# Performance work log

Hardware: AMD Instinct MI355X
Metric: run time of the kernel (lower is better)

## Reference

```python
import math
import jax, jax.numpy as jnp
import numpy as np

D_MODEL = 1024
NUM_HEADS = 16
D_K = D_MODEL // NUM_HEADS
RANK = 16
B, L = 2, 2048


def setup_inputs() -> dict:
    key = jax.random.key(0)
    ks = jax.random.split(key, 10)
    w_scale = 0.02  # keep activations well-scaled like trained linears
    return {
        "x_q": jax.random.normal(ks[0], (B, L, D_MODEL), jnp.float32),
        "x_kv": jax.random.normal(ks[1], (B, L, D_MODEL), jnp.float32),
        "Wq": jax.random.normal(ks[2], (D_MODEL, D_MODEL), jnp.float32) * w_scale,
        "bq": jnp.zeros((D_MODEL,), jnp.float32),
        "Wk": jax.random.normal(ks[3], (D_MODEL, D_MODEL), jnp.float32) * w_scale,
        "bk": jnp.zeros((D_MODEL,), jnp.float32),
        "Wv": jax.random.normal(ks[4], (D_MODEL, D_MODEL), jnp.float32) * w_scale,
        "bv": jnp.zeros((D_MODEL,), jnp.float32),
        "Wo": jax.random.normal(ks[5], (D_MODEL, D_MODEL), jnp.float32) * w_scale,
        "bo": jnp.zeros((D_MODEL,), jnp.float32),
        "U_bil": jax.random.normal(ks[6], (NUM_HEADS, D_K, RANK), jnp.float32) * 0.02,
        "V_bil": jax.random.normal(ks[7], (NUM_HEADS, D_K, RANK), jnp.float32) * 0.02,
        "padding_mask": jnp.zeros((B, L), bool),  # True = padded KV position
    }


def reference(x_q, x_kv, Wq, bq, Wk, bk, Wv, bv, Wo, bo, U_bil, V_bil, padding_mask):
    b, l, _ = x_q.shape
    # torch nn.Linear: y = x @ W.T + b
    Q = (x_q @ Wq.T + bq).reshape(b, l, NUM_HEADS, D_K).transpose(0, 2, 1, 3)  # [B,H,L,dk]
    K = (x_kv @ Wk.T + bk).reshape(b, l, NUM_HEADS, D_K).transpose(0, 2, 1, 3)
    V = (x_kv @ Wv.T + bv).reshape(b, l, NUM_HEADS, D_K).transpose(0, 2, 1, 3)
    # low-rank bilinear projections: [B,H,L,rank]
    Q_proj = jnp.einsum("bhld,hdr->bhlr", Q, U_bil)
    K_proj = jnp.einsum("bhld,hdr->bhlr", K, V_bil)
    scores = jnp.einsum("bhqr,bhkr->bhqk", Q_proj, K_proj) / math.sqrt(RANK)  # [B,H,L,L]
    scores = jnp.where(padding_mask[:, None, None, :], jnp.float32(-10000.0), scores)
    attn = jax.nn.softmax(scores, axis=-1)  # dropout is identity in eval mode
    ctx = jnp.einsum("bhqk,bhkd->bhqd", attn, V)
    ctx = ctx.transpose(0, 2, 1, 3).reshape(b, l, D_MODEL)
    return ctx @ Wo.T + bo
```

## Files before the change

### kernel.cpp

```cpp
#include <hip/hip_runtime.h>
#include <hip/hip_bf16.h>

#define DM   1024
#define NH   16
#define DK   64
#define RK   16
#define BB   2
#define LL   2048
#define TT   (BB*LL)
#define NSPL 2


typedef float f4   __attribute__((ext_vector_type(4)));
typedef float f2   __attribute__((ext_vector_type(2)));
typedef float f16v __attribute__((ext_vector_type(16)));
typedef short s8v  __attribute__((ext_vector_type(8)));
typedef unsigned int u2v __attribute__((ext_vector_type(2)));
typedef unsigned int u4v __attribute__((ext_vector_type(4)));

static __device__ __forceinline__ unsigned short f2b(float f) {
  __hip_bfloat16 h = __float2bfloat16(f);
  unsigned short u;
  __builtin_memcpy(&u, &h, 2);
  return u;
}
static __device__ __forceinline__ float b2f(unsigned short u) {
  __hip_bfloat16 h;
  __builtin_memcpy(&h, &u, 2);
  return __bfloat162float(h);
}

static __device__ __forceinline__ void gld_lds16(const void* g, void* l) {
  __builtin_amdgcn_global_load_lds(
      (const __attribute__((address_space(1))) unsigned int*)g,
      (__attribute__((address_space(3))) unsigned int*)l, 16, 0, 0);
}

static __device__ __forceinline__ void wait_vm0_barrier() {
  asm volatile("s_waitcnt vmcnt(0)" ::: "memory");
  __builtin_amdgcn_s_barrier();
}

static __device__ __forceinline__ void cast_rng(
    const float* __restrict__ s, unsigned short* __restrict__ d,
    int n4, int lb, int nb, int tid) {
  for (int i = lb*256 + tid; i < n4; i += nb*256) {
    const float4 v = ((const float4*)s)[i];
    ushort4 o;
    o.x = f2b(v.x); o.y = f2b(v.y); o.z = f2b(v.z); o.w = f2b(v.w);
    ((ushort4*)d)[i] = o;
  }
}

__global__ __launch_bounds__(256) void prep_k(
    const float* __restrict__ xq,  const float* __restrict__ xkv,
    const float* __restrict__ Wv,  const float* __restrict__ Wo,
    unsigned short* __restrict__ xq_b,  unsigned short* __restrict__ xkv_b,
    unsigned short* __restrict__ Wv_b,  unsigned short* __restrict__ Wo_b,
    const float* __restrict__ Wq,  const float* __restrict__ Wk,
    const float* __restrict__ Uq,  const float* __restrict__ Uk,
    unsigned short* __restrict__ Aq, unsigned short* __restrict__ Ak,
    const float* __restrict__ bq,  const float* __restrict__ bk,
    float* __restrict__ bpq, float* __restrict__ bpk) {
  __shared__ float sh[64*16 + 4*64];
  const int x = blockIdx.x, tid = threadIdx.x;
  if (x < 1024) {
    cast_rng(xq,  xq_b,  TT*DM/4, x,        1024, tid);
  } else if (x < 2048) {
    cast_rng(xkv, xkv_b, TT*DM/4, x - 1024, 1024, tid);
  } else if (x < 2304) {
    cast_rng(Wv,  Wv_b,  DM*DM/4, x - 2048, 256, tid);
  } else if (x < 2560) {
    cast_rng(Wo,  Wo_b,  DM*DM/4, x - 2304, 256, tid);
  } else if (x < 3072) {
    const int fidx = x - 2560;
    const int sel = fidx >> 8, f = fidx & 255;
    const float* W = sel ? Wk : Wq;
    const float* U = sel ? Uk : Uq;
    unsigned short* At = sel ? Ak : Aq;
    const float qs = sel ? 1.f : 0.25f;
    const int i0 = (f & 15) * 64, h = f >> 4;
    float* Us = sh;
    float* Ws = sh + 1024;
    const int il = tid & 63, rr = tid >> 6;
    for (int t = tid; t < 64*16; t += 256)
      Us[t] = U[(size_t)(h*DK + (t >> 4))*RK + (t & 15)];
    float acc[4] = {};
    for (int d0 = 0; d0 < DK; d0 += 4) {
      __syncthreads();
      Ws[rr*64 + il] = W[(size_t)(h*DK + d0 + rr)*DM + i0 + il];
      __syncthreads();
#pragma unroll
      for (int dd = 0; dd < 4; ++dd) {
        const float w = Ws[dd*64 + il];
#pragma unroll
        for (int j = 0; j < 4; ++j)
          acc[j] += w * Us[(d0 + dd)*16 + rr*4 + j];
      }
    }
#pragma unroll
    for (int j = 0; j < 4; ++j)
      At[(size_t)(h*RK + rr*4 + j)*DM + i0 + il] = f2b(acc[j] * qs);
  } else {
    const int h = tid >> 4, r = tid & 15;
    float aq = 0.f, ak = 0.f;
    for (int d = 0; d < DK; ++d) {
      aq += bq[h*DK + d] * Uq[(size_t)(h*DK + d)*RK + r];
      ak += bk[h*DK + d] * Uk[(size_t)(h*DK + d)*RK + r];
    }
    bpq[tid] = aq * 0.25f; bpk[tid] = ak;
  }
}

__global__ __launch_bounds__(256) void proj_k(
    const unsigned short* __restrict__ xq_b, const unsigned short* __restrict__ xkv_b,
    const unsigned short* __restrict__ Atq,  const unsigned short* __restrict__ Atk,
    const float* __restrict__ bpq, const float* __restrict__ bpk,
    unsigned short* __restrict__ Qp, unsigned short* __restrict__ Kp,
    const unsigned short* __restrict__ Wv_b, const float* __restrict__ bv,
    unsigned short* __restrict__ Vt) {
  __shared__ __align__(16) unsigned short shm[16384];
  const int f = blockIdx.x, tid = threadIdx.x;
  const int wave = tid >> 6, lane = tid & 63;
  const int quad = lane >> 4, l15 = lane & 15;
  const int ar = tid >> 2, ac = (tid & 3) * 8;
  const f4 z = {0.f, 0.f, 0.f, 0.f};

  if (f < 256) {
    const int xb = f & 63, yb = (f >> 6) & 1, zb = f >> 7;
    const unsigned short* Ag = zb ? xkv_b : xq_b;
    const unsigned short* Bg = zb ? Atk : Atq;
    const float* bias = zb ? bpk : bpq;
    unsigned short* C = zb ? Kp : Qp;
    unsigned short* Xs = shm;
    unsigned short* Bq = shm + 4096;
    const int t0 = xb*64, n0 = yb*128, nh = wave*32;
    f4 acc[4][2];
#pragma unroll
    for (int a = 0; a < 4; ++a) { acc[a][0] = z; acc[a][1] = z; }

    auto STAGE = [&](int buf, int k0) {
      gld_lds16(&Ag[(size_t)(t0 + ar)*DM + k0 + ac],      &Xs[buf*2048 + wave*512]);
      gld_lds16(&Bg[(size_t)(n0 + ar)*DM + k0 + ac],      &Bq[buf*4096 + wave*512]);
      gld_lds16(&Bg[(size_t)(n0 + 64 + ar)*DM + k0 + ac], &Bq[buf*4096 + 2048 + wave*512]);
    };
    STAGE(0, 0);
    wait_vm0_barrier();
    int cur = 0;
    for (int k0 = 0; k0 < DM; k0 += 32) {
      if (k0 + 32 < DM) STAGE(cur ^ 1, k0 + 32);
      s8v af[4], bf[2];
#pragma unroll
      for (int ms = 0; ms < 4; ++ms)
        af[ms] = *(const s8v*)&Xs[cur*2048 + (ms*16 + l15)*32 + quad*8];
#pragma unroll
      for (int ns = 0; ns < 2; ++ns)
        bf[ns] = *(const s8v*)&Bq[cur*4096 + (nh + ns*16 + l15)*32 + quad*8];
#pragma unroll
      for (int ms = 0; ms < 4; ++ms)
#pragma unroll
        for (int ns = 0; ns < 2; ++ns)
          acc[ms][ns] = __builtin_amdgcn_mfma_f32_16x16x32_bf16(
              af[ms], bf[ns], acc[ms][ns], 0, 0, 0);
      wait_vm0_barrier();
      cur ^= 1;
    }
#pragma unroll
    for (int ms = 0; ms < 4; ++ms) {
      const int tb = t0 + ms*16 + quad*4;
#pragma unroll
      for (int ns = 0; ns < 2; ++ns) {
        const int o = n0 + nh + ns*16 + l15;
        const float bvv = bias[o];
        f4 a = acc[ms][ns];
#pragma unroll
        for (int rg = 0; rg < 4; ++rg) {
          const int tt = tb + rg;
          C[(((size_t)(tt >> 11)*NH + (o >> 4))*LL + (tt & 2047))*RK + (o & 15)]
              = f2b(a[rg] + bvv);
        }
      }
    }
  } else {
    const int g = f - 256, gx = g & 31, gy = g >> 5;
    unsigned short* As = shm;
    unsigned short* Bs = shm + 8192;
    const int t0 = gx*128, n0 = gy*128;
    f4 acc[2][8];
#pragma unroll
    for (int m = 0; m < 2; ++m)
#pragma unroll
      for (int n = 0; n < 8; ++n) acc[m][n] = z;

    auto STAGE = [&](int buf, int k0) {
      gld_lds16(&xkv_b[(size_t)(t0 + ar)*DM + k0 + ac],      &As[buf*4096 + wave*512]);
      gld_lds16(&xkv_b[(size_t)(t0 + 64 + ar)*DM + k0 + ac], &As[buf*4096 + 2048 + wave*512]);
      gld_lds16(&Wv_b[(size_t)(n0 + ar)*DM + k0 + ac],       &Bs[buf*4096 + wave*512]);
      gld_lds16(&Wv_b[(size_t)(n0 + 64 + ar)*DM + k0 + ac],  &Bs[buf*4096 + 2048 + wave*512]);
    };
    STAGE(0, 0);
    wait_vm0_barrier();
    int cur = 0;
    for (int k0 = 0; k0 < DM; k0 += 32) {
      if (k0 + 32 < DM) STAGE(cur ^ 1, k0 + 32);
      s8v af[2], bf[8];
#pragma unroll
      for (int ms = 0; ms < 2; ++ms)
        af[ms] = *(const s8v*)&As[cur*4096 + (wave*32 + ms*16 + l15)*32 + quad*8];
#pragma unroll
      for (int ns = 0; ns < 8; ++ns)
        bf[ns] = *(const s8v*)&Bs[cur*4096 + (ns*16 + l15)*32 + quad*8];
#pragma unroll
      for (int ms = 0; ms < 2; ++ms)
#pragma unroll
        for (int ns = 0; ns < 8; ++ns)
          acc[ms][ns] = __builtin_amdgcn_mfma_f32_16x16x32_bf16(
              af[ms], bf[ns], acc[ms][ns], 0, 0, 0);
      wait_vm0_barrier();
      cur ^= 1;
    }
#pragma unroll
    for (int ms = 0; ms < 2; ++ms) {
      const int tb = t0 + wave*32 + ms*16 + quad*4;
#pragma unroll
      for (int ns = 0; ns < 8; ++ns) {
        const int o = n0 + ns*16 + l15;
        const float bvv = bv[o];
        f4 a = acc[ms][ns];
        const int bb = tb >> 11, l = tb & 2047;
        ushort4 pk;
        pk.x = f2b(a[0] + bvv); pk.y = f2b(a[1] + bvv);
        pk.z = f2b(a[2] + bvv); pk.w = f2b(a[3] + bvv);
        *(ushort4*)&Vt[((size_t)bb*DM + o)*LL + l] = pk;
      }
    }
  }
}

template<bool MASKED>
static __device__ __forceinline__ void softmax_pack(
    const f16v& s0, const f16v& s1, const unsigned long long mb, const int hi,
    f2& den2, unsigned int (&Pd)[2][4][2]) {
  const f2 neg1 = {-1.f, -1.f};
#pragma unroll
  for (int nt = 0; nt < 2; ++nt) {
    const f16v& sv = nt ? s1 : s0;
#pragma unroll
    for (int r = 0; r < 4; ++r) {
#pragma unroll
      for (int jp = 0; jp < 2; ++jp) {
        f2 em2;
        em2[0] = __expf(sv[r*4 + jp*2]);
        em2[1] = __expf(sv[r*4 + jp*2 + 1]);
        if (MASKED) {
          const int kl = nt*32 + jp*2 + 8*r + 4*hi;
          if ((mb >> kl) & 1ull)       em2[0] = 0.f;
          if ((mb >> (kl + 1)) & 1ull) em2[1] = 0.f;
        }
        f2 ep2;
        asm("v_pk_add_f32 %0, %1, %2" : "=v"(ep2) : "v"(em2), "v"(neg1));
        asm("v_pk_add_f32 %0, %0, %1" : "+v"(den2) : "v"(ep2));
        asm("v_cvt_pk_bf16_f32 %0, %1, %2"
            : "=v"(Pd[nt][r][jp]) : "v"(ep2[0]), "v"(ep2[1]));
      }
    }
  }
}

__global__ __launch_bounds__(256, 4) void attn_k(
    const unsigned short* __restrict__ Qp, const unsigned short* __restrict__ Kp,
    const unsigned short* __restrict__ Vt,
    const unsigned char* __restrict__ msk,
    unsigned short* __restrict__ P, float* __restrict__ denP,
    float* __restrict__ Vsum) {
  __shared__ __align__(16) unsigned short Ks[2][2][65][8];
  __shared__ __align__(16) unsigned short Vs[2][8][65][8];
  const int tid = threadIdx.x;

  if (blockIdx.z == 4) {
    if (blockIdx.y >= BB) return;
    const int h = blockIdx.x, b = blockIdx.y;
    const int d = tid >> 2, part = tid & 3;
    const unsigned short* row = Vt + ((size_t)b*DM + h*DK + d)*LL + part*512;
    float s = 0.f;
    for (int i = 0; i < 512; i += 8) {
      const s8v v = *(const s8v*)&row[i];
#pragma unroll
      for (int j = 0; j < 8; ++j) s += b2f((unsigned short)v[j]);
    }
    s += __shfl_xor(s, 1);
    s += __shfl_xor(s, 2);
    if (part == 0) Vsum[((size_t)b*NH + h)*DK + d] = s;
    return;
  }

  const int q0 = blockIdx.x * 128, h = blockIdx.y;
  const int b = blockIdx.z & (BB - 1), ksp = blockIdx.z >> 1;
  const int kbeg = ksp * (LL / NSPL);
  const int NT = (LL / NSPL) / 64;
  const int w = tid >> 6, lane = tid & 63;
  const int l31 = lane & 31, hi = lane >> 5;

  const s8v qfrag = *(const s8v*)&Qp[
      (((size_t)b*NH + h)*LL + q0 + w*32 + l31)*RK + hi*8];

  const int sr = tid >> 2, sp = tid & 3;
  const unsigned short* __restrict__ Vrow =
      Vt + ((size_t)b*DM + h*DK + sr)*LL + kbeg;
  const unsigned short* __restrict__ Kbase =
      Kp + (((size_t)b*NH + h)*LL + kbeg + sr)*RK + sp*4;
  const unsigned char*  __restrict__ Mrow = msk + (size_t)b*LL + kbeg + lane;

  u2v kpre; s8v vpre0, vpre1;
  unsigned char mcur, mnext;

  kpre  = *(const u2v*)&Kbase[0];
  vpre0 = *(const s8v*)&Vrow[sp*16];
  vpre1 = *(const s8v*)&Vrow[sp*16 + 8];
  mcur  = Mrow[0];
  *(u2v*)&Ks[0][sp>>1][sr][(sp&1)*4] = kpre;
  *(s8v*)&Vs[0][sp*2][sr][0]   = vpre0;
  *(s8v*)&Vs[0][sp*2+1][sr][0] = vpre1;
  kpre  = *(const u2v*)&Kbase[(size_t)64*RK];
  vpre0 = *(const s8v*)&Vrow[64 + sp*16];
  vpre1 = *(const s8v*)&Vrow[64 + sp*16 + 8];
  mnext = Mrow[64];
  __syncthreads();

  f16v acc0, acc1, z16;
#pragma unroll
  for (int i = 0; i < 16; ++i) { acc0[i] = 0.f; acc1[i] = 0.f; z16[i] = 0.f; }
  f2 den2 = {0.f, 0.f};

  for (int t = 0; t < NT; ++t) {
    const int cur = t & 1;
    const unsigned long long mb = __ballot(mcur != 0);

    const s8v kf0 = *(const s8v*)&Ks[cur][hi][l31][0];
    const s8v kf1 = *(const s8v*)&Ks[cur][hi][32 + l31][0];

    const f16v s0 = __builtin_amdgcn_mfma_f32_32x32x16_bf16(kf0, qfrag, z16, 0, 0, 0);
    const f16v s1 = __builtin_amdgcn_mfma_f32_32x32x16_bf16(kf1, qfrag, z16, 0, 0, 0);

    unsigned int Pd[2][4][2];
    if (__builtin_expect(mb != 0ull, 0))
      softmax_pack<true >(s0, s1, mb, hi, den2, Pd);
    else
      softmax_pack<false>(s0, s1, mb, hi, den2, Pd);

#pragma unroll
    for (int kc = 0; kc < 4; ++kc) {
      const int nt = kc >> 1, a = (kc & 1)*2;
      const u2v r0 = __builtin_amdgcn_permlane32_swap(
          Pd[nt][a][0], Pd[nt][a+1][0], false, false);
      const u2v r1 = __builtin_amdgcn_permlane32_swap(
          Pd[nt][a][1], Pd[nt][a+1][1], false, false);
      u4v efi;
      efi[0] = r0[0];
      efi[1] = r1[0];
      efi[2] = r0[1];
      efi[3] = r1[1];
      const s8v ef = __builtin_bit_cast(s8v, efi);
      const s8v vf0 = *(const s8v*)&Vs[cur][kc*2 + hi][l31][0];
      const s8v vf1 = *(const s8v*)&Vs[cur][kc*2 + hi][32 + l31][0];
      acc0 = __builtin_amdgcn_mfma_f32_32x32x16_bf16(ef, vf0, acc0, 0, 0, 0);
      acc1 = __builtin_amdgcn_mfma_f32_32x32x16_bf16(ef, vf1, acc1, 0, 0, 0);
    }

    if (t + 1 < NT) {
      *(u2v*)&Ks[cur^1][sp>>1][sr][(sp&1)*4] = kpre;
      *(s8v*)&Vs[cur^1][sp*2][sr][0]   = vpre0;
      *(s8v*)&Vs[cur^1][sp*2+1][sr][0] = vpre1;
      const int tn = (t + 2 < NT) ? t + 2 : NT - 1;
      kpre  = *(const u2v*)&Kbase[(size_t)tn*64*RK];
      vpre0 = *(const s8v*)&Vrow[tn*64 + sp*16];
      vpre1 = *(const s8v*)&Vrow[tn*64 + sp*16 + 8];
      mcur  = mnext;
      mnext = Mrow[tn*64];
    }
    __syncthreads();
  }

  float den = den2[0] + den2[1] + (float)(32 * NT);
  den += __shfl_xor(den, 32);
  if (hi == 0)
    denP[(((size_t)ksp*BB + b)*NH + h)*LL + q0 + w*32 + l31] = den;

#pragma unroll
  for (int rg = 0; rg < 16; ++rg) {
    const int qr = (rg & 3) + 8*(rg >> 2) + 4*hi;
    const size_t pbase =
        ((size_t)ksp*TT + b*LL + q0 + w*32 + qr)*DM + h*DK;
    P[pbase + l31]      = f2b(acc0[rg]);
    P[pbase + 32 + l31] = f2b(acc1[rg]);
  }
}

__global__ __launch_bounds__(256) void outred_k(
    const unsigned short* __restrict__ P, const float* __restrict__ Vsum,
    const float* __restrict__ denP, const unsigned short* __restrict__ Bg,
    const float* __restrict__ bias, float* __restrict__ C) {
  __shared__ __align__(16) unsigned short P0s[2][2048];
  __shared__ __align__(16) unsigned short P1s[2][2048];
  __shared__ __align__(16) unsigned short Bs[2][4096];
  __shared__ float vsS[1024];
  __shared__ float invS[64][16];
  const int f = blockIdx.x;
  const int t0 = (f & 63) * 64, n0 = (f >> 6) * 128;
  const int tid = threadIdx.x, wave = tid >> 6, lane = tid & 63;
  const int quad = lane >> 4, l15 = lane & 15;
  const int nh = wave * 32;
  const int ar = tid >> 2, ac = (tid & 3) * 8;
  const int trow = t0 + ar;
  const int b = t0 >> 11;

  for (int i = tid; i < 1024; i += 256)
    vsS[i] = Vsum[(size_t)b*DM + i];
  {
    const int r = tid >> 2, h0 = (tid & 3) * 4;
    const int lr = (t0 + r) & 2047;
#pragma unroll
    for (int j = 0; j < 4; ++j) {
      const int h = h0 + j;
      const float dn = denP[((size_t)b*NH + h)*LL + lr] +
                       denP[(((size_t)BB + b)*NH + h)*LL + lr];
      invS[r][h] = 1.f / fmaxf(dn, 1e-30f);
    }
  }

  auto STAGE = [&](int buf, int k0) {
    gld_lds16(&P[(size_t)trow*DM + k0 + ac],             &P0s[buf][wave*512]);
    gld_lds16(&P[((size_t)TT + trow)*DM + k0 + ac],      &P1s[buf][wave*512]);
    gld_lds16(&Bg[(size_t)(n0 + ar)*DM + k0 + ac],       &Bs[buf][wave*512]);
    gld_lds16(&Bg[(size_t)(n0 + 64 + ar)*DM + k0 + ac],  &Bs[buf][2048 + wave*512]);
  };
  STAGE(0, 0);
  asm volatile("s_waitcnt vmcnt(0) lgkmcnt(0)" ::: "memory");
  __builtin_amdgcn_s_barrier();

  const f4 z = {0.f, 0.f, 0.f, 0.f};
  f4 acc[4][2];
#pragma unroll
  for (int a = 0; a < 4; ++a) { acc[a][0] = z; acc[a][1] = z; }

  int cur = 0;
  for (int k0 = 0; k0 < DM; k0 += 32) {
    if (k0 + 32 < DM) STAGE(cur ^ 1, k0 + 32);
    const int hk = k0 >> 6;
    const f4 vq0 = *(const f4*)&vsS[k0 + quad*8];
    const f4 vq1 = *(const f4*)&vsS[k0 + quad*8 + 4];
    s8v af[4], bf[2];
#pragma unroll
    for (int ms = 0; ms < 4; ++ms) {
      const int r16 = ms*16 + l15;
      const float inv = invS[r16][hk];
      const s8v p0 = *(const s8v*)&P0s[cur][r16*32 + quad*8];
      const s8v p1 = *(const s8v*)&P1s[cur][r16*32 + quad*8];
      float e[8];
#pragma unroll
      for (int j = 0; j < 4; ++j) {
        e[j]     = (vq0[j] + b2f((unsigned short)p0[j])
                           + b2f((unsigned short)p1[j])) * inv;
        e[4 + j] = (vq1[j] + b2f((unsigned short)p0[4+j])
                           + b2f((unsigned short)p1[4+j])) * inv;
      }
      unsigned int d0, d1, d2, d3;
      asm("v_cvt_pk_bf16_f32 %0, %1, %2" : "=v"(d0) : "v"(e[0]), "v"(e[1]));
      asm("v_cvt_pk_bf16_f32 %0, %1, %2" : "=v"(d1) : "v"(e[2]), "v"(e[3]));
      asm("v_cvt_pk_bf16_f32 %0, %1, %2" : "=v"(d2) : "v"(e[4]), "v"(e[5]));
      asm("v_cvt_pk_bf16_f32 %0, %1, %2" : "=v"(d3) : "v"(e[6]), "v"(e[7]));
      u4v efi; efi[0] = d0; efi[1] = d1; efi[2] = d2; efi[3] = d3;
      af[ms] = __builtin_bit_cast(s8v, efi);
    }
#pragma unroll
    for (int ns = 0; ns < 2; ++ns)
      bf[ns] = *(const s8v*)&Bs[cur][(nh + ns*16 + l15)*32 + quad*8];
#pragma unroll
    for (int ms = 0; ms < 4; ++ms)
#pragma unroll
      for (int ns = 0; ns < 2; ++ns)
        acc[ms][ns] = __builtin_amdgcn_mfma_f32_16x16x32_bf16(
            af[ms], bf[ns], acc[ms][ns], 0, 0, 0);
    wait_vm0_barrier();
    cur ^= 1;
  }

#pragma unroll
  for (int ms = 0; ms < 4; ++ms) {
    const int tb = t0 + ms*16 + quad*4;
#pragma unroll
    for (int ns = 0; ns < 2; ++ns) {
      const int o = n0 + nh + ns*16 + l15;
      const float bv = bias[o];
      f4 a = acc[ms][ns];
#pragma unroll
      for (int rg = 0; rg < 4; ++rg)
        C[(size_t)(tb + rg)*DM + o] = a[rg] + bv;
    }
  }
}

extern "C" void kernel_launch(void* const* d_in, const int* in_sizes, int n_in,
                              void* d_out, int out_size, void* d_ws, size_t ws_size,
                              hipStream_t stream) {
  (void)in_sizes; (void)n_in; (void)out_size; (void)ws_size;
  const float* x_q   = (const float*)d_in[0];
  const float* x_kv  = (const float*)d_in[1];
  const float* Wq    = (const float*)d_in[2];
  const float* bq    = (const float*)d_in[3];
  const float* Wk    = (const float*)d_in[4];
  const float* bk    = (const float*)d_in[5];
  const float* Wv    = (const float*)d_in[6];
  const float* bv    = (const float*)d_in[7];
  const float* Wo    = (const float*)d_in[8];
  const float* bo    = (const float*)d_in[9];
  const float* U_bil = (const float*)d_in[10];
  const float* V_bil = (const float*)d_in[11];
  const unsigned char* pmask = (const unsigned char*)d_in[12];
  float* out = (float*)d_out;

  char* w = (char*)d_ws;
  unsigned short* xq_b  = (unsigned short*)(w);
  unsigned short* xkv_b = (unsigned short*)(w +  8388608);
  unsigned short* Wv_b  = (unsigned short*)(w + 16777216);
  unsigned short* Wo_b  = (unsigned short*)(w + 18874368);
  unsigned short* Atq   = (unsigned short*)(w + 20971520);
  unsigned short* Atk   = (unsigned short*)(w + 21495808);
  float*          bpq   = (float*)(w + 22020096);
  float*          bpk   = (float*)(w + 22021120);
  unsigned short* Qp    = (unsigned short*)(w + 22022144);
  unsigned short* Kp    = (unsigned short*)(w + 24119296);
  unsigned short* Vt    = (unsigned short*)(w + 26216448);
  float*          Vsum  = (float*)(w + 34605056);
  float*          denP  = (float*)(w + 34613248);
  unsigned short* Pbuf  = (unsigned short*)w;

  prep_k<<<3073, 256, 0, stream>>>(
      x_q, x_kv, Wv, Wo, xq_b, xkv_b, Wv_b, Wo_b,
      Wq, Wk, U_bil, V_bil, Atq, Atk, bq, bk, bpq, bpk);
  proj_k<<<512, 256, 0, stream>>>(
      xq_b, xkv_b, Atq, Atk, bpq, bpk, Qp, Kp, Wv_b, bv, Vt);
  attn_k<<<dim3(LL/128, NH, 5), 256, 0, stream>>>(
      Qp, Kp, Vt, pmask, Pbuf, denP, Vsum);
  outred_k<<<512, 256, 0, stream>>>(Pbuf, Vsum, denP, Wo_b, bo, out);
}
```

Before: 227.3 us.

## Fuse all stages into one cooperative persistent kernel with grid syncs

Merges the four kernels (cast/prep, projection, attention, output reduction) into a single cooperative kernel of 1024 blocks separated by grid.sync(), with a multi-launch fallback. The aim is to remove launch gaps and tail effects between stages. To fit four blocks per CU it drops the double-buffered LDS staging in favour of single-buffer loads with two __syncthreads per k-step. It also retiles the V projection to 64x128 tiles, switches softmax to raw v_exp_f32 with the log2e factor folded into the Q scale, and transposes the denominator layout so it can be read as vectors.

```diff
diff --git a/kernel.cpp b/kernel.cpp
--- a/kernel.cpp
+++ b/kernel.cpp
@@ -1,5 +1,8 @@
 #include <hip/hip_runtime.h>
 #include <hip/hip_bf16.h>
+#include <hip/hip_cooperative_groups.h>
+
+namespace cg = cooperative_groups;
 
 #define DM   1024
 #define NH   16
@@ -18,6 +21,15 @@
 typedef unsigned int u2v __attribute__((ext_vector_type(2)));
 typedef unsigned int u4v __attribute__((ext_vector_type(4)));
 
+#define SMEM_BYTES 24576
+
+struct Args {
+  const float *xq, *xkv, *Wv, *Wo, *Wq, *Wk, *Uq, *Uk, *bq, *bk, *bv, *bo;
+  const unsigned char* msk;
+  unsigned short *xq_b, *xkv_b, *Wv_b, *Wo_b, *Atq, *Atk, *Qp, *Kp, *Vt, *P;
+  float *bpq, *bpk, *denP, *Vsum, *out;
+};
+
 static __device__ __forceinline__ unsigned short f2b(float f) {
   __hip_bfloat16 h = __float2bfloat16(f);
   unsigned short u;
@@ -29,6 +41,9 @@
   __builtin_memcpy(&h, &u, 2);
   return __bfloat162float(h);
 }
+static __device__ __forceinline__ float fexp2(float x) {
+  float r; asm("v_exp_f32 %0, %1" : "=v"(r) : "v"(x)); return r;
+}
 
 static __device__ __forceinline__ void gld_lds16(const void* g, void* l) {
   __builtin_amdgcn_global_load_lds(
@@ -36,52 +51,32 @@
       (__attribute__((address_space(3))) unsigned int*)l, 16, 0, 0);
 }
 
-static __device__ __forceinline__ void wait_vm0_barrier() {
-  asm volatile("s_waitcnt vmcnt(0)" ::: "memory");
-  __builtin_amdgcn_s_barrier();
-}
-
-static __device__ __forceinline__ void cast_rng(
-    const float* __restrict__ s, unsigned short* __restrict__ d,
-    int n4, int lb, int nb, int tid) {
-  for (int i = lb*256 + tid; i < n4; i += nb*256) {
-    const float4 v = ((const float4*)s)[i];
+#define QSCALE 0.36067376022224085f
+
+static __device__ void stage_prep(char* sm, int id, const Args& a) {
+  const int tid = threadIdx.x;
+  const int NF = TT*DM/4, NW = DM*DM/4;
+  const int TOTC = 2*NF + 2*NW;
+  for (int i = id*256 + tid; i < TOTC; i += 1024*256) {
+    const float* s; unsigned short* d; int off;
+    if (i < NF)           { s = a.xq;  d = a.xq_b;  off = i; }
+    else if (i < 2*NF)    { s = a.xkv; d = a.xkv_b; off = i - NF; }
+    else if (i < 2*NF+NW) { s = a.Wv;  d = a.Wv_b;  off = i - 2*NF; }
+    else                  { s = a.Wo;  d = a.Wo_b;  off = i - 2*NF - NW; }
+    const float4 v = ((const float4*)s)[off];
     ushort4 o;
     o.x = f2b(v.x); o.y = f2b(v.y); o.z = f2b(v.z); o.w = f2b(v.w);
-    ((ushort4*)d)[i] = o;
-  }
-}
-
-__global__ __launch_bounds__(256) void prep_k(
-    const float* __restrict__ xq,  const float* __restrict__ xkv,
-    const float* __restrict__ Wv,  const float* __restrict__ Wo,
-    unsigned short* __restrict__ xq_b,  unsigned short* __restrict__ xkv_b,
-    unsigned short* __restrict__ Wv_b,  unsigned short* __restrict__ Wo_b,
-    const float* __restrict__ Wq,  const float* __restrict__ Wk,
-    const float* __restrict__ Uq,  const float* __restrict__ Uk,
-    unsigned short* __restrict__ Aq, unsigned short* __restrict__ Ak,
-    const float* __restrict__ bq,  const float* __restrict__ bk,
-    float* __restrict__ bpq, float* __restrict__ bpk) {
-  __shared__ float sh[64*16 + 4*64];
-  const int x = blockIdx.x, tid = threadIdx.x;
-  if (x < 1024) {
-    cast_rng(xq,  xq_b,  TT*DM/4, x,        1024, tid);
-  } else if (x < 2048) {
-    cast_rng(xkv, xkv_b, TT*DM/4, x - 1024, 1024, tid);
-  } else if (x < 2304) {
-    cast_rng(Wv,  Wv_b,  DM*DM/4, x - 2048, 256, tid);
-  } else if (x < 2560) {
-    cast_rng(Wo,  Wo_b,  DM*DM/4, x - 2304, 256, tid);
-  } else if (x < 3072) {
-    const int fidx = x - 2560;
-    const int sel = fidx >> 8, f = fidx & 255;
-    const float* W = sel ? Wk : Wq;
-    const float* U = sel ? Uk : Uq;
-    unsigned short* At = sel ? Ak : Aq;
-    const float qs = sel ? 1.f : 0.25f;
+    ((ushort4*)d)[off] = o;
+  }
+  if (id < 512) {
+    const int sel = id >> 8, f = id & 255;
+    const float* W = sel ? a.Wk : a.Wq;
+    const float* U = sel ? a.Uk : a.Uq;
+    unsigned short* At = sel ? a.Atk : a.Atq;
+    const float qs = sel ? 1.f : QSCALE;
     const int i0 = (f & 15) * 64, h = f >> 4;
-    float* Us = sh;
-    float* Ws = sh + 1024;
+    float* Us = (float*)sm;
+    float* Ws = (float*)sm + 1024;
     const int il = tid & 63, rr = tid >> 6;
     for (int t = tid; t < 64*16; t += 256)
       Us[t] = U[(size_t)(h*DK + (t >> 4))*RK + (t & 15)];
@@ -101,69 +96,57 @@
 #pragma unroll
     for (int j = 0; j < 4; ++j)
       At[(size_t)(h*RK + rr*4 + j)*DM + i0 + il] = f2b(acc[j] * qs);
-  } else {
+  } else if (id == 512) {
     const int h = tid >> 4, r = tid & 15;
     float aq = 0.f, ak = 0.f;
     for (int d = 0; d < DK; ++d) {
-      aq += bq[h*DK + d] * Uq[(size_t)(h*DK + d)*RK + r];
-      ak += bk[h*DK + d] * Uk[(size_t)(h*DK + d)*RK + r];
-    }
-    bpq[tid] = aq * 0.25f; bpk[tid] = ak;
-  }
-}
-
-__global__ __launch_bounds__(256) void proj_k(
-    const unsigned short* __restrict__ xq_b, const unsigned short* __restrict__ xkv_b,
-    const unsigned short* __restrict__ Atq,  const unsigned short* __restrict__ Atk,
-    const float* __restrict__ bpq, const float* __restrict__ bpk,
-    unsigned short* __restrict__ Qp, unsigned short* __restrict__ Kp,
-    const unsigned short* __restrict__ Wv_b, const float* __restrict__ bv,
-    unsigned short* __restrict__ Vt) {
-  __shared__ __align__(16) unsigned short shm[16384];
-  const int f = blockIdx.x, tid = threadIdx.x;
+      aq += a.bq[h*DK + d] * a.Uq[(size_t)(h*DK + d)*RK + r];
+      ak += a.bk[h*DK + d] * a.Uk[(size_t)(h*DK + d)*RK + r];
+    }
+    a.bpq[tid] = aq * QSCALE;
+    a.bpk[tid] = ak;
+  }
+}
+
+static __device__ void stage_proj(char* sm, int id, const Args& a) {
+  if (id >= 768) return;
+  const int tid = threadIdx.x;
   const int wave = tid >> 6, lane = tid & 63;
   const int quad = lane >> 4, l15 = lane & 15;
   const int ar = tid >> 2, ac = (tid & 3) * 8;
   const f4 z = {0.f, 0.f, 0.f, 0.f};
-
-  if (f < 256) {
-    const int xb = f & 63, yb = (f >> 6) & 1, zb = f >> 7;
-    const unsigned short* Ag = zb ? xkv_b : xq_b;
-    const unsigned short* Bg = zb ? Atk : Atq;
-    const float* bias = zb ? bpk : bpq;
-    unsigned short* C = zb ? Kp : Qp;
-    unsigned short* Xs = shm;
-    unsigned short* Bq = shm + 4096;
+  unsigned short* Xs = (unsigned short*)sm;
+  unsigned short* Bs = (unsigned short*)(sm + 4096);
+
+  if (id < 256) {
+    const int xb = id & 63, yb = (id >> 6) & 1, zb = id >> 7;
+    const unsigned short* Ag = zb ? a.xkv_b : a.xq_b;
+    const unsigned short* Bg = zb ? a.Atk : a.Atq;
+    const float* bias = zb ? a.bpk : a.bpq;
+    unsigned short* C = zb ? a.Kp : a.Qp;
     const int t0 = xb*64, n0 = yb*128, nh = wave*32;
     f4 acc[4][2];
 #pragma unroll
-    for (int a = 0; a < 4; ++a) { acc[a][0] = z; acc[a][1] = z; }
-
-    auto STAGE = [&](int buf, int k0) {
-      gld_lds16(&Ag[(size_t)(t0 + ar)*DM + k0 + ac],      &Xs[buf*2048 + wave*512]);
-      gld_lds16(&Bg[(size_t)(n0 + ar)*DM + k0 + ac],      &Bq[buf*4096 + wave*512]);
-      gld_lds16(&Bg[(size_t)(n0 + 64 + ar)*DM + k0 + ac], &Bq[buf*4096 + 2048 + wave*512]);
-    };
-    STAGE(0, 0);
-    wait_vm0_barrier();
-    int cur = 0;
+    for (int q = 0; q < 4; ++q) { acc[q][0] = z; acc[q][1] = z; }
     for (int k0 = 0; k0 < DM; k0 += 32) {
-      if (k0 + 32 < DM) STAGE(cur ^ 1, k0 + 32);
+      __syncthreads();
+      gld_lds16(&Ag[(size_t)(t0 + ar)*DM + k0 + ac],      &Xs[wave*512]);
+      gld_lds16(&Bg[(size_t)(n0 + ar)*DM + k0 + ac],      &Bs[wave*512]);
+      gld_lds16(&Bg[(size_t)(n0 + 64 + ar)*DM + k0 + ac], &Bs[2048 + wave*512]);
+      __syncthreads();
       s8v af[4], bf[2];
 #pragma unroll
       for (int ms = 0; ms < 4; ++ms)
-        af[ms] = *(const s8v*)&Xs[cur*2048 + (ms*16 + l15)*32 + quad*8];
+        af[ms] = *(const s8v*)&Xs[(ms*16 + l15)*32 + quad*8];
 #pragma unroll
       for (int ns = 0; ns < 2; ++ns)
-        bf[ns] = *(const s8v*)&Bq[cur*4096 + (nh + ns*16 + l15)*32 + quad*8];
+        bf[ns] = *(const s8v*)&Bs[(nh + ns*16 + l15)*32 + quad*8];
 #pragma unroll
       for (int ms = 0; ms < 4; ++ms)
 #pragma unroll
         for (int ns = 0; ns < 2; ++ns)
           acc[ms][ns] = __builtin_amdgcn_mfma_f32_16x16x32_bf16(
               af[ms], bf[ns], acc[ms][ns], 0, 0, 0);
-      wait_vm0_barrier();
-      cur ^= 1;
     }
 #pragma unroll
     for (int ms = 0; ms < 4; ++ms) {
@@ -172,66 +155,54 @@
       for (int ns = 0; ns < 2; ++ns) {
         const int o = n0 + nh + ns*16 + l15;
         const float bvv = bias[o];
-        f4 a = acc[ms][ns];
+        f4 v = acc[ms][ns];
 #pragma unroll
         for (int rg = 0; rg < 4; ++rg) {
           const int tt = tb + rg;
           C[(((size_t)(tt >> 11)*NH + (o >> 4))*LL + (tt & 2047))*RK + (o & 15)]
-              = f2b(a[rg] + bvv);
+              = f2b(v[rg] + bvv);
         }
       }
     }
   } else {
-    const int g = f - 256, gx = g & 31, gy = g >> 5;
-    unsigned short* As = shm;
-    unsigned short* Bs = shm + 8192;
-    const int t0 = gx*128, n0 = gy*128;
-    f4 acc[2][8];
-#pragma unroll
-    for (int m = 0; m < 2; ++m)
-#pragma unroll
-      for (int n = 0; n < 8; ++n) acc[m][n] = z;
-
-    auto STAGE = [&](int buf, int k0) {
-      gld_lds16(&xkv_b[(size_t)(t0 + ar)*DM + k0 + ac],      &As[buf*4096 + wave*512]);
-      gld_lds16(&xkv_b[(size_t)(t0 + 64 + ar)*DM + k0 + ac], &As[buf*4096 + 2048 + wave*512]);
-      gld_lds16(&Wv_b[(size_t)(n0 + ar)*DM + k0 + ac],       &Bs[buf*4096 + wave*512]);
-      gld_lds16(&Wv_b[(size_t)(n0 + 64 + ar)*DM + k0 + ac],  &Bs[buf*4096 + 2048 + wave*512]);
-    };
-    STAGE(0, 0);
-    wait_vm0_barrier();
-    int cur = 0;
+    const int g = id - 256;
+    const int t0 = (g & 63)*64, n0 = (g >> 6)*128, nh = wave*32;
+    f4 acc[4][2];
+#pragma unroll
+    for (int q = 0; q < 4; ++q) { acc[q][0] = z; acc[q][1] = z; }
     for (int k0 = 0; k0 < DM; k0 += 32) {
-      if (k0 + 32 < DM) STAGE(cur ^ 1, k0 + 32);
-      s8v af[2], bf[8];
-#pragma unroll
-      for (int ms = 0; ms < 2; ++ms)
-        af[ms] = *(const s8v*)&As[cur*4096 + (wave*32 + ms*16 + l15)*32 + quad*8];
-#pragma unroll
-      for (int ns = 0; ns < 8; ++ns)
-        bf[ns] = *(const s8v*)&Bs[cur*4096 + (ns*16 + l15)*32 + quad*8];
-#pragma unroll
-      for (int ms = 0; ms < 2; ++ms)
-#pragma unroll
-        for (int ns = 0; ns < 8; ++ns)
+      __syncthreads();
+      gld_lds16(&a.xkv_b[(size_t)(t0 + ar)*DM + k0 + ac],     &Xs[wave*512]);
+      gld_lds16(&a.Wv_b[(size_t)(n0 + ar)*DM + k0 + ac],      &Bs[wave*512]);
+      gld_lds16(&a.Wv_b[(size_t)(n0 + 64 + ar)*DM + k0 + ac], &Bs[2048 + wave*512]);
+      __syncthreads();
+      s8v af[4], bf[2];
+#pragma unroll
+      for (int ms = 0; ms < 4; ++ms)
+        af[ms] = *(const s8v*)&Xs[(ms*16 + l15)*32 + quad*8];
+#pragma unroll
+      for (int ns = 0; ns < 2; ++ns)
+        bf[ns] = *(const s8v*)&Bs[(nh + ns*16 + l15)*32 + quad*8];
+#pragma unroll
+      for (int ms = 0; ms < 4; ++ms)
+#pragma unroll
+        for (int ns = 0; ns < 2; ++ns)
           acc[ms][ns] = __builtin_amdgcn_mfma_f32_16x16x32_bf16(
               af[ms], bf[ns], acc[ms][ns], 0, 0, 0);
-      wait_vm0_barrier();
-      cur ^= 1;
-    }
-#pragma unroll
-    for (int ms = 0; ms < 2; ++ms) {
-      const int tb = t0 + wave*32 + ms*16 + quad*4;
-#pragma unroll
-      for (int ns = 0; ns < 8; ++ns) {
-        const int o = n0 + ns*16 + l15;
-        const float bvv = bv[o];
-        f4 a = acc[ms][ns];
+    }
+#pragma unroll
+    for (int ms = 0; ms < 4; ++ms) {
+      const int tb = t0 + ms*16 + quad*4;
+#pragma unroll
+      for (int ns = 0; ns < 2; ++ns) {
+        const int o = n0 + nh + ns*16 + l15;
+        const float bvv = a.bv[o];
+        f4 v = acc[ms][ns];
         const int bb = tb >> 11, l = tb & 2047;
         ushort4 pk;
-        pk.x = f2b(a[0] + bvv); pk.y = f2b(a[1] + bvv);
-        pk.z = f2b(a[2] + bvv); pk.w = f2b(a[3] + bvv);
-        *(ushort4*)&Vt[((size_t)bb*DM + o)*LL + l] = pk;
+        pk.x = f2b(v[0] + bvv); pk.y = f2b(v[1] + bvv);
+        pk.z = f2b(v[2] + bvv); pk.w = f2b(v[3] + bvv);
+        *(ushort4*)&a.Vt[((size_t)bb*DM + o)*LL + l] = pk;
       }
     }
   }
@@ -250,8 +221,8 @@
 #pragma unroll
       for (int jp = 0; jp < 2; ++jp) {
         f2 em2;
-        em2[0] = __expf(sv[r*4 + jp*2]);
-        em2[1] = __expf(sv[r*4 + jp*2 + 1]);
+        em2[0] = fexp2(sv[r*4 + jp*2]);
+        em2[1] = fexp2(sv[r*4 + jp*2 + 1]);
         if (MASKED) {
           const int kl = nt*32 + jp*2 + 8*r + 4*hi;
           if ((mb >> kl) & 1ull)       em2[0] = 0.f;
@@ -267,49 +238,28 @@
   }
 }
 
-__global__ __launch_bounds__(256, 4) void attn_k(
-    const unsigned short* __restrict__ Qp, const unsigned short* __restrict__ Kp,
-    const unsigned short* __restrict__ Vt,
-    const unsigned char* __restrict__ msk,
-    unsigned short* __restrict__ P, float* __restrict__ denP,
-    float* __restrict__ Vsum) {
-  __shared__ __align__(16) unsigned short Ks[2][2][65][8];
-  __shared__ __align__(16) unsigned short Vs[2][8][65][8];
+static __device__ void stage_attn(char* sm, int id, const Args& a) {
   const int tid = threadIdx.x;
-
-  if (blockIdx.z == 4) {
-    if (blockIdx.y >= BB) return;
-    const int h = blockIdx.x, b = blockIdx.y;
-    const int d = tid >> 2, part = tid & 3;
-    const unsigned short* row = Vt + ((size_t)b*DM + h*DK + d)*LL + part*512;
-    float s = 0.f;
-    for (int i = 0; i < 512; i += 8) {
-      const s8v v = *(const s8v*)&row[i];
-#pragma unroll
-      for (int j = 0; j < 8; ++j) s += b2f((unsigned short)v[j]);
-    }
-    s += __shfl_xor(s, 1);
-    s += __shfl_xor(s, 2);
-    if (part == 0) Vsum[((size_t)b*NH + h)*DK + d] = s;
-    return;
-  }
-
-  const int q0 = blockIdx.x * 128, h = blockIdx.y;
-  const int b = blockIdx.z & (BB - 1), ksp = blockIdx.z >> 1;
+  auto Ks = (unsigned short (*)[2][65][8])sm;
+  auto Vs = (unsigned short (*)[8][65][8])(sm + 4160);
+
+  const int q0 = (id & 15) * 128, h = (id >> 4) & 15;
+  const int zz = id >> 8;
+  const int b = zz & (BB - 1), ksp = zz >> 1;
   const int kbeg = ksp * (LL / NSPL);
   const int NT = (LL / NSPL) / 64;
   const int w = tid >> 6, lane = tid & 63;
   const int l31 = lane & 31, hi = lane >> 5;
 
-  const s8v qfrag = *(const s8v*)&Qp[
+  const s8v qfrag = *(const s8v*)&a.Qp[
       (((size_t)b*NH + h)*LL + q0 + w*32 + l31)*RK + hi*8];
 
   const int sr = tid >> 2, sp = tid & 3;
   const unsigned short* __restrict__ Vrow =
-      Vt + ((size_t)b*DM + h*DK + sr)*LL + kbeg;
+      a.Vt + ((size_t)b*DM + h*DK + sr)*LL + kbeg;
   const unsigned short* __restrict__ Kbase =
-      Kp + (((size_t)b*NH + h)*LL + kbeg + sr)*RK + sp*4;
-  const unsigned char*  __restrict__ Mrow = msk + (size_t)b*LL + kbeg + lane;
+      a.Kp + (((size_t)b*NH + h)*LL + kbeg + sr)*RK + sp*4;
+  const unsigned char*  __restrict__ Mrow = a.msk + (size_t)b*LL + kbeg + lane;
 
   u2v kpre; s8v vpre0, vpre1;
   unsigned char mcur, mnext;
@@ -350,11 +300,11 @@
 
 #pragma unroll
     for (int kc = 0; kc < 4; ++kc) {
-      const int nt = kc >> 1, a = (kc & 1)*2;
+      const int nt = kc >> 1, aa = (kc & 1)*2;
       const u2v r0 = __builtin_amdgcn_permlane32_swap(
-          Pd[nt][a][0], Pd[nt][a+1][0], false, false);
+          Pd[nt][aa][0], Pd[nt][aa+1][0], false, false);
       const u2v r1 = __builtin_amdgcn_permlane32_swap(
-          Pd[nt][a][1], Pd[nt][a+1][1], false, false);
+          Pd[nt][aa][1], Pd[nt][aa+1][1], false, false);
       u4v efi;
       efi[0] = r0[0];
       efi[1] = r1[0];
@@ -384,30 +334,45 @@
   float den = den2[0] + den2[1] + (float)(32 * NT);
   den += __shfl_xor(den, 32);
   if (hi == 0)
-    denP[(((size_t)ksp*BB + b)*NH + h)*LL + q0 + w*32 + l31] = den;
+    a.denP[(((size_t)b*LL + q0 + w*32 + l31)*NSPL + ksp)*NH + h] = den;
 
 #pragma unroll
   for (int rg = 0; rg < 16; ++rg) {
     const int qr = (rg & 3) + 8*(rg >> 2) + 4*hi;
     const size_t pbase =
         ((size_t)ksp*TT + b*LL + q0 + w*32 + qr)*DM + h*DK;
-    P[pbase + l31]      = f2b(acc0[rg]);
-    P[pbase + 32 + l31] = f2b(acc1[rg]);
-  }
-}
-
-__global__ __launch_bounds__(256) void outred_k(
-    const unsigned short* __restrict__ P, const float* __restrict__ Vsum,
-    const float* __restrict__ denP, const unsigned short* __restrict__ Bg,
-    const float* __restrict__ bias, float* __restrict__ C) {
-  __shared__ __align__(16) unsigned short P0s[2][2048];
-  __shared__ __align__(16) unsigned short P1s[2][2048];
-  __shared__ __align__(16) unsigned short Bs[2][4096];
-  __shared__ float vsS[1024];
-  __shared__ float invS[64][16];
-  const int f = blockIdx.x;
-  const int t0 = (f & 63) * 64, n0 = (f >> 6) * 128;
-  const int tid = threadIdx.x, wave = tid >> 6, lane = tid & 63;
+    a.P[pbase + l31]      = f2b(acc0[rg]);
+    a.P[pbase + 32 + l31] = f2b(acc1[rg]);
+  }
+
+  if (id < 32) {
+    const int vh = id & 15, vb = id >> 4;
+    const int d = tid >> 2, part = tid & 3;
+    const unsigned short* row =
+        a.Vt + ((size_t)vb*DM + vh*DK + d)*LL + part*512;
+    float s = 0.f;
+    for (int i = 0; i < 512; i += 8) {
+      const s8v v = *(const s8v*)&row[i];
+#pragma unroll
+      for (int j = 0; j < 8; ++j) s += b2f((unsigned short)v[j]);
+    }
+    s += __shfl_xor(s, 1);
+    s += __shfl_xor(s, 2);
+    if (part == 0) a.Vsum[((size_t)vb*NH + vh)*DK + d] = s;
+  }
+}
+
+static __device__ void stage_outred(char* sm, int id, const Args& a) {
+  if (id >= 512) return;
+  const int tid = threadIdx.x;
+  unsigned short* P0s = (unsigned short*)sm;
+  unsigned short* P1s = (unsigned short*)(sm + 4096);
+  unsigned short* Bss = (unsigned short*)(sm + 8192);
+  float* vsS  = (float*)(sm + 16384);
+  float* invS = (float*)(sm + 20480);
+
+  const int t0 = (id & 63) * 64, n0 = (id >> 6) * 128;
+  const int wave = tid >> 6, lane = tid & 63;
   const int quad = lane >> 4, l15 = lane & 15;
   const int nh = wave * 32;
   const int ar = tid >> 2, ac = (tid & 3) * 8;
@@ -415,37 +380,30 @@
   const int b = t0 >> 11;
 
   for (int i = tid; i < 1024; i += 256)
-    vsS[i] = Vsum[(size_t)b*DM + i];
+    vsS[i] = a.Vsum[(size_t)b*DM + i];
   {
     const int r = tid >> 2, h0 = (tid & 3) * 4;
-    const int lr = (t0 + r) & 2047;
-#pragma unroll
-    for (int j = 0; j < 4; ++j) {
-      const int h = h0 + j;
-      const float dn = denP[((size_t)b*NH + h)*LL + lr] +
-                       denP[(((size_t)BB + b)*NH + h)*LL + lr];
-      invS[r][h] = 1.f / fmaxf(dn, 1e-30f);
-    }
-  }
-
-  auto STAGE = [&](int buf, int k0) {
-    gld_lds16(&P[(size_t)trow*DM + k0 + ac],             &P0s[buf][wave*512]);
-    gld_lds16(&P[((size_t)TT + trow)*DM + k0 + ac],      &P1s[buf][wave*512]);
-    gld_lds16(&Bg[(size_t)(n0 + ar)*DM + k0 + ac],       &Bs[buf][wave*512]);
-    gld_lds16(&Bg[(size_t)(n0 + 64 + ar)*DM + k0 + ac],  &Bs[buf][2048 + wave*512]);
-  };
-  STAGE(0, 0);
-  asm volatile("s_waitcnt vmcnt(0) lgkmcnt(0)" ::: "memory");
-  __builtin_amdgcn_s_barrier();
+    const size_t base = (size_t)(t0 + r) * (NSPL*NH);
+    const f4 d0 = *(const f4*)&a.denP[base + h0];
+    const f4 d1 = *(const f4*)&a.denP[base + NH + h0];
+#pragma unroll
+    for (int j = 0; j < 4; ++j)
+      invS[r*16 + h0 + j] = 1.f / fmaxf(d0[j] + d1[j], 1e-30f);
+  }
 
   const f4 z = {0.f, 0.f, 0.f, 0.f};
   f4 acc[4][2];
 #pragma unroll
-  for (int a = 0; a < 4; ++a) { acc[a][0] = z; acc[a][1] = z; }
-
-  int cur = 0;
+  for (int q = 0; q < 4; ++q) { acc[q][0] = z; acc[q][1] = z; }
+
   for (int k0 = 0; k0 < DM; k0 += 32) {
-    if (k0 + 32 < DM) STAGE(cur ^ 1, k0 + 32);
+    __syncthreads();
+    gld_lds16(&a.P[(size_t)trow*DM + k0 + ac],              &P0s[wave*512]);
+    gld_lds16(&a.P[((size_t)TT + trow)*DM + k0 + ac],       &P1s[wave*512]);
+    gld_lds16(&a.Wo_b[(size_t)(n0 + ar)*DM + k0 + ac],      &Bss[wave*512]);
+    gld_lds16(&a.Wo_b[(size_t)(n0 + 64 + ar)*DM + k0 + ac], &Bss[2048 + wave*512]);
+    __syncthreads();
+
     const int hk = k0 >> 6;
     const f4 vq0 = *(const f4*)&vsS[k0 + quad*8];
     const f4 vq1 = *(const f4*)&vsS[k0 + quad*8 + 4];
@@ -453,9 +411,9 @@
 #pragma unroll
     for (int ms = 0; ms < 4; ++ms) {
       const int r16 = ms*16 + l15;
-      const float inv = invS[r16][hk];
-      const s8v p0 = *(const s8v*)&P0s[cur][r16*32 + quad*8];
-      const s8v p1 = *(const s8v*)&P1s[cur][r16*32 + quad*8];
+      const float inv = invS[r16*16 + hk];
+      const s8v p0 = *(const s8v*)&P0s[r16*32 + quad*8];
+      const s8v p1 = *(const s8v*)&P1s[r16*32 + quad*8];
       float e[8];
 #pragma unroll
       for (int j = 0; j < 4; ++j) {
@@ -474,15 +432,13 @@
     }
 #pragma unroll
     for (int ns = 0; ns < 2; ++ns)
-      bf[ns] = *(const s8v*)&Bs[cur][(nh + ns*16 + l15)*32 + quad*8];
+      bf[ns] = *(const s8v*)&Bss[(nh + ns*16 + l15)*32 + quad*8];
 #pragma unroll
     for (int ms = 0; ms < 4; ++ms)
 #pragma unroll
       for (int ns = 0; ns < 2; ++ns)
         acc[ms][ns] = __builtin_amdgcn_mfma_f32_16x16x32_bf16(
             af[ms], bf[ns], acc[ms][ns], 0, 0, 0);
-    wait_vm0_barrier();
-    cur ^= 1;
   }
 
 #pragma unroll
@@ -491,56 +447,95 @@
 #pragma unroll
     for (int ns = 0; ns < 2; ++ns) {
       const int o = n0 + nh + ns*16 + l15;
-      const float bv = bias[o];
-      f4 a = acc[ms][ns];
+      const float bvv = a.bo[o];
+      f4 v = acc[ms][ns];
 #pragma unroll
       for (int rg = 0; rg < 4; ++rg)
-        C[(size_t)(tb + rg)*DM + o] = a[rg] + bv;
-    }
-  }
+        a.out[(size_t)(tb + rg)*DM + o] = v[rg] + bvv;
+    }
+  }
+}
+
+__global__ __launch_bounds__(256, 4) void fused_all(Args a) {
+  __shared__ __align__(16) char sm[SMEM_BYTES];
+  cg::grid_group grid = cg::this_grid();
+  const int id = blockIdx.x;
+  stage_prep(sm, id, a);
+  grid.sync();
+  stage_proj(sm, id, a);
+  grid.sync();
+  stage_attn(sm, id, a);
+  grid.sync();
+  stage_outred(sm, id, a);
+}
+
+__global__ __launch_bounds__(256, 4) void prep_w(Args a) {
+  __shared__ __align__(16) char sm[SMEM_BYTES];
+  stage_prep(sm, blockIdx.x, a);
+}
+__global__ __launch_bounds__(256, 4) void proj_w(Args a) {
+  __shared__ __align__(16) char sm[SMEM_BYTES];
+  stage_proj(sm, blockIdx.x, a);
+}
+__global__ __launch_bounds__(256, 4) void attn_w(Args a) {
+  __shared__ __align__(16) char sm[SMEM_BYTES];
+  stage_attn(sm, blockIdx.x, a);
+}
+__global__ __launch_bounds__(256, 4) void outred_w(Args a) {
+  __shared__ __align__(16) char sm[SMEM_BYTES];
+  stage_outred(sm, blockIdx.x, a);
 }
 
 extern "C" void kernel_launch(void* const* d_in, const int* in_sizes, int n_in,
                               void* d_out, int out_size, void* d_ws, size_t ws_size,
                               hipStream_t stream) {
   (void)in_sizes; (void)n_in; (void)out_size; (void)ws_size;
-  const float* x_q   = (const float*)d_in[0];
-  const float* x_kv  = (const float*)d_in[1];
-  const float* Wq    = (const float*)d_in[2];
-  const float* bq    = (const float*)d_in[3];
-  const float* Wk    = (const float*)d_in[4];
-  const float* bk    = (const float*)d_in[5];
-  const float* Wv    = (const float*)d_in[6];
-  const float* bv    = (const float*)d_in[7];
-  const float* Wo    = (const float*)d_in[8];
-  const float* bo    = (const float*)d_in[9];
-  const float* U_bil = (const float*)d_in[10];
-  const float* V_bil = (const float*)d_in[11];
-  const unsigned char* pmask = (const unsigned char*)d_in[12];
-  float* out = (float*)d_out;
-
   char* w = (char*)d_ws;
-  unsigned short* xq_b  = (unsigned short*)(w);
-  unsigned short* xkv_b = (unsigned short*)(w +  8388608);
-  unsigned short* Wv_b  = (unsigned short*)(w + 16777216);
-  unsigned short* Wo_b  = (unsigned short*)(w + 18874368);
-  unsigned short* Atq   = (unsigned short*)(w + 20971520);
-  unsigned short* Atk   = (unsigned short*)(w + 21495808);
-  float*          bpq   = (float*)(w + 22020096);
-  float*          bpk   = (float*)(w + 22021120);
-  unsigned short* Qp    = (unsigned short*)(w + 22022144);
-  unsigned short* Kp    = (unsigned short*)(w + 24119296);
-  unsigned short* Vt    = (unsigned short*)(w + 26216448);
-  float*          Vsum  = (float*)(w + 34605056);
-  float*          denP  = (float*)(w + 34613248);
-  unsigned short* Pbuf  = (unsigned short*)w;
-
-  prep_k<<<3073, 256, 0, stream>>>(
-      x_q, x_kv, Wv, Wo, xq_b, xkv_b, Wv_b, Wo_b,
-      Wq, Wk, U_bil, V_bil, Atq, Atk, bq, bk, bpq, bpk);
-  proj_k<<<512, 256, 0, stream>>>(
-      xq_b, xkv_b, Atq, Atk, bpq, bpk, Qp, Kp, Wv_b, bv, Vt);
-  attn_k<<<dim3(LL/128, NH, 5), 256, 0, stream>>>(
-      Qp, Kp, Vt, pmask, Pbuf, denP, Vsum);
-  outred_k<<<512, 256, 0, stream>>>(Pbuf, Vsum, denP, Wo_b, bo, out);
-}
+  Args a;
+  a.xq    = (const float*)d_in[0];
+  a.xkv   = (const float*)d_in[1];
+  a.Wq    = (const float*)d_in[2];
+  a.bq    = (const float*)d_in[3];
+  a.Wk    = (const float*)d_in[4];
+  a.bk    = (const float*)d_in[5];
+  a.Wv    = (const float*)d_in[6];
+  a.bv    = (const float*)d_in[7];
+  a.Wo    = (const float*)d_in[8];
+  a.bo    = (const float*)d_in[9];
+  a.Uq    = (const float*)d_in[10];
+  a.Uk    = (const float*)d_in[11];
+  a.msk   = (const unsigned char*)d_in[12];
+  a.xq_b  = (unsigned short*)(w);
+  a.xkv_b = (unsigned short*)(w +  8388608);
+  a.Wv_b  = (unsigned short*)(w + 16777216);
+  a.Wo_b  = (unsigned short*)(w + 18874368);
+  a.Atq   = (unsigned short*)(w + 20971520);
+  a.Atk   = (unsigned short*)(w + 21495808);
+  a.bpq   = (float*)(w + 22020096);
+  a.bpk   = (float*)(w + 22021120);
+  a.Qp    = (unsigned short*)(w + 22022144);
+  a.Kp    = (unsigned short*)(w + 24119296);
+  a.Vt    = (unsigned short*)(w + 26216448);
+  a.Vsum  = (float*)(w + 34605056);
+  a.denP  = (float*)(w + 34613248);
+  a.P     = (unsigned short*)w;
+  a.out   = (float*)d_out;
+
+  int dev = 0, coop = 0, ncu = 0, nblk = 0;
+  hipGetDevice(&dev);
+  hipDeviceGetAttribute(&coop, hipDeviceAttributeCooperativeLaunch, dev);
+  hipDeviceGetAttribute(&ncu, hipDeviceAttributeMultiprocessorCount, dev);
+  hipOccupancyMaxActiveBlocksPerMultiprocessor(
+      &nblk, (const void*)fused_all, 256, 0);
+
+  if (coop && (long)nblk * ncu >= 1024) {
+    void* kargs[] = {(void*)&a};
+    hipLaunchCooperativeKernel((const void*)fused_all,
+                               dim3(1024), dim3(256), kargs, 0, stream);
+  } else {
+    prep_w<<<1024, 256, 0, stream>>>(a);
+    proj_w<<<768, 256, 0, stream>>>(a);
+    attn_w<<<1024, 256, 0, stream>>>(a);
+    outred_w<<<512, 256, 0, stream>>>(a);
+  }
+}
```

After: 229.2 us. Within noise of the previous version (+0.8%).
